# Kernel tuning notes

Measured on AMD Instinct MI355X. Metric: run time of the kernel, lower is better.

Reference implementation:

```python
import jax, jax.numpy as jnp
import numpy as np
from jax import lax

K = 8        # num neighbors (excluding self)
ALPHA = 0.5
EPS = 1e-12


def setup_inputs() -> dict:
    key = jax.random.key(0)
    k1, k2 = jax.random.split(key)
    B, N = 4, 4096
    pred = jax.random.normal(k1, (B, N, 3), dtype=jnp.float32)
    target = jax.random.normal(k2, (B, N, 3), dtype=jnp.float32)
    return {"pred": pred, "target": target}


def _pdist(x):
    # x: [B, N, 3] -> Euclidean distance matrix [B, N, N]
    sq = jnp.sum(x * x, axis=-1)                                # [B, N]
    d2 = sq[:, :, None] + sq[:, None, :] - 2.0 * jnp.einsum('bnd,bmd->bnm', x, x)
    return jnp.sqrt(jnp.maximum(d2, EPS))


def _knn_idx(dist, k):
    # smallest k+1 distances, drop self (first column)
    _, idx = lax.top_k(-dist, k + 1)                            # [B, N, k+1]
    return idx[:, :, 1:]                                        # [B, N, k]


def _gather_points(pts, idx):
    # pts: [B, N, 3], idx: [B, N, k] -> [B, N, k, 3]
    return jax.vmap(lambda p, i: p[i])(pts, idx)


def reference(pred, target):
    # Per-batch losses are means over equal-size point sets, so averaging over
    # (B, N) jointly is identical to the original per-batch loop + /B.
    pred_dist = _pdist(pred)
    target_dist = _pdist(target)
    pred_idx = _knn_idx(pred_dist, K)
    target_idx = _knn_idx(target_dist, K)

    # density: mean kNN distance per point
    pred_density = jnp.mean(jnp.take_along_axis(pred_dist, pred_idx, axis=2), axis=2)
    target_density = jnp.mean(jnp.take_along_axis(target_dist, target_idx, axis=2), axis=2)
    density_loss = jnp.mean((pred_density - target_density) ** 2)

    # direction similarity of normalized neighbor offsets
    pred_nb = _gather_points(pred, pred_idx)                    # [B, N, K, 3]
    target_nb = _gather_points(target, target_idx)
    pred_vec = pred_nb - pred[:, :, None, :]
    target_vec = target_nb - target[:, :, None, :]
    pn = pred_vec / jnp.maximum(jnp.linalg.norm(pred_vec, axis=-1, keepdims=True), EPS)
    tn = target_vec / jnp.maximum(jnp.linalg.norm(target_vec, axis=-1, keepdims=True), EPS)
    direction_loss = 1.0 - jnp.mean(jnp.sum(pn * tn, axis=-1))

    # local covariance (curvature proxy)
    pred_cov = jnp.einsum('bnki,bnkj->bnij', pred_vec, pred_vec) / K    # [B, N, 3, 3]
    target_cov = jnp.einsum('bnki,bnkj->bnij', target_vec, target_vec) / K
    cov_diff = jnp.sqrt(jnp.sum((pred_cov - target_cov) ** 2, axis=(-2, -1)))
    curvature_loss = jnp.mean(cov_diff)

    return density_loss + ALPHA * direction_loss + (1.0 - ALPHA) * curvature_loss
```

## Files before the change

kernel.cpp:

```cpp
#include <hip/hip_runtime.h>
#include <cstdint>
#include <cstddef>

#define NPTS   4096
#define BATCH  4
#define KNN    8
#define NC     16
#define CHN    (NPTS / NC)
#define PD     4
#define EPS_F  1e-12f

__device__ __forceinline__ uint32_t u32min(uint32_t a, uint32_t b) { return a < b ? a : b; }
__device__ __forceinline__ uint32_t u32max(uint32_t a, uint32_t b) { return a > b ? a : b; }

__device__ __forceinline__ uint32_t umed3(uint32_t a, uint32_t b, uint32_t c) {
  uint32_t d;
  asm("v_med3_u32 %0, %1, %2, %3" : "=v"(d) : "v"(a), "v"(b), "v"(c));
  return d;
}

template <int D>
__device__ __forceinline__ void insertD(uint32_t (&loc)[D], uint32_t key) {
  uint32_t prev = loc[0];
  loc[0] = u32min(prev, key);
#pragma unroll
  for (int m = 1; m < D; ++m) {
    const uint32_t cur = loc[m];
    loc[m] = umed3(prev, cur, key);
    prev = cur;
  }
}

template <int D>
__device__ __forceinline__ void scan_chunk(const float4* __restrict__ c4, int j0,
                                           float xix, float xiy, float xiz,
                                           uint32_t (&loc)[D]) {
#pragma unroll
  for (int k = 0; k < D; ++k) loc[k] = 0xFFFFFFFFu;
#pragma unroll 4
  for (int t4 = 0; t4 < CHN / 4; ++t4) {
    const float4 q0 = c4[3 * t4 + 0];
    const float4 q1 = c4[3 * t4 + 1];
    const float4 q2 = c4[3 * t4 + 2];
    const uint32_t jb = (uint32_t)(j0 + 4 * t4);
    {
      const float dx = xix - q0.x, dy = xiy - q0.y, dz = xiz - q0.z;
      const float d2 = fmaf(dx, dx, fmaf(dy, dy, dz * dz));
      insertD<D>(loc, (__float_as_uint(d2) & 0xFFFFF000u) | (jb + 0u));
    }
    {
      const float dx = xix - q0.w, dy = xiy - q1.x, dz = xiz - q1.y;
      const float d2 = fmaf(dx, dx, fmaf(dy, dy, dz * dz));
      insertD<D>(loc, (__float_as_uint(d2) & 0xFFFFF000u) | (jb + 1u));
    }
    {
      const float dx = xix - q1.z, dy = xiy - q1.w, dz = xiz - q2.x;
      const float d2 = fmaf(dx, dx, fmaf(dy, dy, dz * dz));
      insertD<D>(loc, (__float_as_uint(d2) & 0xFFFFF000u) | (jb + 2u));
    }
    {
      const float dx = xix - q2.y, dy = xiy - q2.z, dz = xiz - q2.w;
      const float d2 = fmaf(dx, dx, fmaf(dy, dy, dz * dz));
      insertD<D>(loc, (__float_as_uint(d2) & 0xFFFFF000u) | (jb + 3u));
    }
  }
}

__global__ void __launch_bounds__(256, 4)
knn_partial_k(const float* __restrict__ pred, const float* __restrict__ tgt,
              uint32_t* __restrict__ partial, double* __restrict__ acc,
              uint32_t* __restrict__ ticket) {
  if (blockIdx.x == 0 && threadIdx.x == 0) {
    acc[0] = 0.0; acc[1] = 0.0; acc[2] = 0.0;
    *ticket = 0u;
  }

  int bx = blockIdx.x;
  const int chunk = bx & (NC - 1); bx /= NC;
  const int ig    = bx & 15; bx >>= 4;
  const int b     = bx & 3;  bx >>= 2;
  const int cloud = bx;

  const float* __restrict__ pts = (cloud ? tgt : pred) + (size_t)b * NPTS * 3;
  const int tid = threadIdx.x;
  const int i = ig * 256 + tid;
  const int j0 = chunk * CHN;

  const float xix = pts[3 * i + 0];
  const float xiy = pts[3 * i + 1];
  const float xiz = pts[3 * i + 2];

  const float4* __restrict__ c4 = (const float4*)(pts + 3 * j0);

  uint4 o;
  if (ig == chunk) {
    uint32_t loc[PD + 1];
    scan_chunk<PD + 1>(c4, j0, xix, xiy, xiz, loc);
    o = make_uint4(loc[1], loc[2], loc[3], loc[4]);
  } else {
    uint32_t loc[PD];
    scan_chunk<PD>(c4, j0, xix, xiy, xiz, loc);
    o = make_uint4(loc[0], loc[1], loc[2], loc[3]);
  }
  uint32_t* p = partial +
      ((((size_t)(cloud * BATCH + b) * NC + chunk) * NPTS) + (size_t)i) * PD;
  *(uint4*)p = o;
}

__device__ __forceinline__ void merge2(uint32_t A[KNN], const uint32_t B[KNN]) {
  uint32_t t[KNN];
#pragma unroll
  for (int m = 0; m < KNN; ++m) t[m] = u32min(A[m], B[KNN - 1 - m]);
#define CEU(x, y) { uint32_t lo = u32min(t[x], t[y]); uint32_t hi = u32max(t[x], t[y]); t[x] = lo; t[y] = hi; }
  CEU(0,4) CEU(1,5) CEU(2,6) CEU(3,7)
  CEU(0,2) CEU(1,3) CEU(4,6) CEU(5,7)
  CEU(0,1) CEU(2,3) CEU(4,5) CEU(6,7)
#undef CEU
#pragma unroll
  for (int m = 0; m < KNN; ++m) A[m] = t[m];
}

__device__ __forceinline__ void merge44(const uint2 a0, const uint2 a1,
                                        const uint2 b0, const uint2 b1,
                                        uint32_t s[KNN]) {
  s[0] = a0.x; s[1] = a0.y; s[2] = a1.x; s[3] = a1.y;
  s[4] = b1.y; s[5] = b1.x; s[6] = b0.y; s[7] = b0.x;
#define CEU(x, y) { uint32_t lo = u32min(s[x], s[y]); uint32_t hi = u32max(s[x], s[y]); s[x] = lo; s[y] = hi; }
  CEU(0,4) CEU(1,5) CEU(2,6) CEU(3,7)
  CEU(0,2) CEU(1,3) CEU(4,6) CEU(5,7)
  CEU(0,1) CEU(2,3) CEU(4,5) CEU(6,7)
#undef CEU
}

__device__ __forceinline__ void merge_all(const uint32_t* __restrict__ base,
                                          int i, uint32_t v[KNN]) {
  const size_t stride = (size_t)NPTS * PD;
  const uint32_t* p = base + (size_t)i * PD;
  uint2 q[NC][2];
#pragma unroll
  for (int c = 0; c < NC; ++c) {
    q[c][0] = *(const uint2*)(p + (size_t)c * stride);
    q[c][1] = *(const uint2*)(p + (size_t)c * stride + 2);
  }
  uint32_t L[NC / 2][KNN];
#pragma unroll
  for (int c = 0; c < NC / 2; ++c)
    merge44(q[2 * c][0], q[2 * c][1], q[2 * c + 1][0], q[2 * c + 1][1], L[c]);
  merge2(L[0], L[1]); merge2(L[2], L[3]); merge2(L[4], L[5]); merge2(L[6], L[7]);
  merge2(L[0], L[2]); merge2(L[4], L[6]);
  merge2(L[0], L[4]);
#pragma unroll
  for (int m = 0; m < KNN; ++m) v[m] = L[0][m];
}

__device__ __forceinline__ void cloud_stats(const float* __restrict__ C, int i,
                                            const uint32_t v[KNN],
                                            float& dsum, float cov[6],
                                            float nx[KNN], float ny[KNN], float nz[KNN]) {
  const float qx = C[3 * i], qy = C[3 * i + 1], qz = C[3 * i + 2];
  float jx[KNN], jy[KNN], jz[KNN];
#pragma unroll
  for (int k = 0; k < KNN; ++k) {
    const int j = (int)(v[k] & 0xFFFu);
    jx[k] = C[3 * j]; jy[k] = C[3 * j + 1]; jz[k] = C[3 * j + 2];
  }
  dsum = 0.f;
#pragma unroll
  for (int m = 0; m < 6; ++m) cov[m] = 0.f;
#pragma unroll
  for (int k = 0; k < KNN; ++k) {
    const float ax = jx[k] - qx, ay = jy[k] - qy, az = jz[k] - qz;
    const float d2 = fmaf(ax, ax, fmaf(ay, ay, az * az));
    const float dist = sqrtf(fmaxf(d2, EPS_F));
    const float inv = 1.0f / fmaxf(dist, EPS_F);
    dsum += dist;
    cov[0] += ax * ax; cov[1] += ay * ay; cov[2] += az * az;
    cov[3] += ax * ay; cov[4] += ax * az; cov[5] += ay * az;
    nx[k] = ax * inv; ny[k] = ay * inv; nz[k] = az * inv;
  }
}

__global__ void __launch_bounds__(64, 1)
loss_k(const float* __restrict__ pred, const float* __restrict__ tgt,
       const uint32_t* __restrict__ partial, double* __restrict__ acc,
       uint32_t* __restrict__ ticket, float* __restrict__ out) {
  const int p = blockIdx.x * 64 + threadIdx.x;
  const int b = p >> 12;
  const int i = p & (NPTS - 1);

  const float* __restrict__ P = pred + (size_t)b * NPTS * 3;
  const float* __restrict__ T = tgt  + (size_t)b * NPTS * 3;

  const size_t cstride = (size_t)NC * NPTS * PD;
  uint32_t vp[KNN], vt[KNN];
  merge_all(partial + (size_t)(0 * BATCH + b) * cstride, i, vp);
  merge_all(partial + (size_t)(1 * BATCH + b) * cstride, i, vt);

  float dsp, dst, pcov[6], tcov[6];
  float pnx[KNN], pny[KNN], pnz[KNN], tnx[KNN], tny[KNN], tnz[KNN];
  cloud_stats(P, i, vp, dsp, pcov, pnx, pny, pnz);
  cloud_stats(T, i, vt, dst, tcov, tnx, tny, tnz);

  float sdot = 0.f;
#pragma unroll
  for (int k = 0; k < KNN; ++k)
    sdot += pnx[k] * tnx[k] + pny[k] * tny[k] + pnz[k] * tnz[k];

  const float densp = dsp * (1.0f / KNN);
  const float denst = dst * (1.0f / KNN);
  float e = (densp - denst) * (densp - denst);

  const float dxx = (pcov[0] - tcov[0]) * (1.0f / KNN);
  const float dyy = (pcov[1] - tcov[1]) * (1.0f / KNN);
  const float dzz = (pcov[2] - tcov[2]) * (1.0f / KNN);
  const float dxy = (pcov[3] - tcov[3]) * (1.0f / KNN);
  const float dxz = (pcov[4] - tcov[4]) * (1.0f / KNN);
  const float dyz = (pcov[5] - tcov[5]) * (1.0f / KNN);
  float cfro = sqrtf(dxx * dxx + dyy * dyy + dzz * dzz
                     + 2.0f * (dxy * dxy + dxz * dxz + dyz * dyz));
  float s = sdot;

#pragma unroll
  for (int off = 32; off > 0; off >>= 1) {
    e    += __shfl_down(e, off);
    s    += __shfl_down(s, off);
    cfro += __shfl_down(cfro, off);
  }
  if (threadIdx.x == 0) {
    atomicAdd(&acc[0], (double)e);
    atomicAdd(&acc[1], (double)s);
    atomicAdd(&acc[2], (double)cfro);
    __threadfence();
    const unsigned rank = atomicAdd(ticket, 1u) + 1u;
    if (rank == (unsigned)((BATCH * NPTS) / 64)) {
      __threadfence();
      const double ee = __hip_atomic_load(&acc[0], __ATOMIC_RELAXED, __HIP_MEMORY_SCOPE_AGENT);
      const double ss = __hip_atomic_load(&acc[1], __ATOMIC_RELAXED, __HIP_MEMORY_SCOPE_AGENT);
      const double cc = __hip_atomic_load(&acc[2], __ATOMIC_RELAXED, __HIP_MEMORY_SCOPE_AGENT);
      const double BN = (double)BATCH * (double)NPTS;
      out[0] = (float)(ee / BN + 0.5 * (1.0 - ss / (BN * (double)KNN)) + 0.5 * (cc / BN));
    }
  }
}

extern "C" void kernel_launch(void* const* d_in, const int* in_sizes, int n_in,
                              void* d_out, int out_size, void* d_ws, size_t ws_size,
                              hipStream_t stream) {
  const float* pred = (const float*)d_in[0];
  const float* tgt  = (const float*)d_in[1];
  double* acc = (double*)d_ws;
  uint32_t* ticket = (uint32_t*)((char*)d_ws + 64);
  uint32_t* partial = (uint32_t*)((char*)d_ws + 4096);

  knn_partial_k<<<2 * BATCH * (NPTS / 256) * NC, 256, 0, stream>>>(
      pred, tgt, partial, acc, ticket);
  loss_k<<<(BATCH * NPTS) / 64, 64, 0, stream>>>(
      pred, tgt, partial, acc, ticket, (float*)d_out);
}
```

Baseline: 106.1 us.

## Transpose points to SoA and use packed FP32 math for kNN distances

Adds a pre-pass kernel that converts each point cloud from AoS xyz into separate X/Y/Z arrays in workspace, and moves the accumulator reset into it. The distance scan then loads float4 groups per axis and computes two squared distances at a time with v_pk_add/mul/fma_f32, roughly halving VALU instructions for the distance arithmetic. The cost is an extra kernel launch and a small transpose pass, and the insertion network, likely the dominant cost, is left unchanged.

```diff
diff --git a/kernel.cpp b/kernel.cpp
--- a/kernel.cpp
+++ b/kernel.cpp
@@ -10,6 +10,8 @@
 #define PD     4
 #define EPS_F  1e-12f
 
+typedef float f32x2 __attribute__((ext_vector_type(2)));
+
 __device__ __forceinline__ uint32_t u32min(uint32_t a, uint32_t b) { return a < b ? a : b; }
 __device__ __forceinline__ uint32_t u32max(uint32_t a, uint32_t b) { return a > b ? a : b; }
 
@@ -19,6 +21,22 @@
   return d;
 }
 
+__device__ __forceinline__ f32x2 pk_add(f32x2 a, f32x2 b) {
+  f32x2 d;
+  asm("v_pk_add_f32 %0, %1, %2" : "=v"(d) : "v"(a), "v"(b));
+  return d;
+}
+__device__ __forceinline__ f32x2 pk_mul(f32x2 a, f32x2 b) {
+  f32x2 d;
+  asm("v_pk_mul_f32 %0, %1, %2" : "=v"(d) : "v"(a), "v"(b));
+  return d;
+}
+__device__ __forceinline__ f32x2 pk_fma(f32x2 a, f32x2 b, f32x2 c) {
+  f32x2 d;
+  asm("v_pk_fma_f32 %0, %1, %2, %3" : "=v"(d) : "v"(a), "v"(b), "v"(c));
+  return d;
+}
+
 template <int D>
 __device__ __forceinline__ void insertD(uint32_t (&loc)[D], uint32_t key) {
   uint32_t prev = loc[0];
@@ -31,50 +49,69 @@
   }
 }
 
-template <int D>
-__device__ __forceinline__ void scan_chunk(const float4* __restrict__ c4, int j0,
-                                           float xix, float xiy, float xiz,
-                                           uint32_t (&loc)[D]) {
-#pragma unroll
-  for (int k = 0; k < D; ++k) loc[k] = 0xFFFFFFFFu;
-#pragma unroll 4
-  for (int t4 = 0; t4 < CHN / 4; ++t4) {
-    const float4 q0 = c4[3 * t4 + 0];
-    const float4 q1 = c4[3 * t4 + 1];
-    const float4 q2 = c4[3 * t4 + 2];
-    const uint32_t jb = (uint32_t)(j0 + 4 * t4);
-    {
-      const float dx = xix - q0.x, dy = xiy - q0.y, dz = xiz - q0.z;
-      const float d2 = fmaf(dx, dx, fmaf(dy, dy, dz * dz));
-      insertD<D>(loc, (__float_as_uint(d2) & 0xFFFFF000u) | (jb + 0u));
-    }
-    {
-      const float dx = xix - q0.w, dy = xiy - q1.x, dz = xiz - q1.y;
-      const float d2 = fmaf(dx, dx, fmaf(dy, dy, dz * dz));
-      insertD<D>(loc, (__float_as_uint(d2) & 0xFFFFF000u) | (jb + 1u));
-    }
-    {
-      const float dx = xix - q1.z, dy = xiy - q1.w, dz = xiz - q2.x;
-      const float d2 = fmaf(dx, dx, fmaf(dy, dy, dz * dz));
-      insertD<D>(loc, (__float_as_uint(d2) & 0xFFFFF000u) | (jb + 2u));
-    }
-    {
-      const float dx = xix - q2.y, dy = xiy - q2.z, dz = xiz - q2.w;
-      const float d2 = fmaf(dx, dx, fmaf(dy, dy, dz * dz));
-      insertD<D>(loc, (__float_as_uint(d2) & 0xFFFFF000u) | (jb + 3u));
-    }
-  }
-}
-
-__global__ void __launch_bounds__(256, 4)
-knn_partial_k(const float* __restrict__ pred, const float* __restrict__ tgt,
-              uint32_t* __restrict__ partial, double* __restrict__ acc,
-              uint32_t* __restrict__ ticket) {
+__global__ void __launch_bounds__(256)
+pre_k(const float* __restrict__ pred, const float* __restrict__ tgt,
+      float* __restrict__ soa, double* __restrict__ acc,
+      uint32_t* __restrict__ ticket) {
   if (blockIdx.x == 0 && threadIdx.x == 0) {
     acc[0] = 0.0; acc[1] = 0.0; acc[2] = 0.0;
     *ticket = 0u;
   }
-
+  const int idx = blockIdx.x * 256 + threadIdx.x;
+  const int cb = idx / (3 * NPTS);
+  const int e  = idx - cb * 3 * NPTS;
+  const int axis = e / NPTS;
+  const int j    = e - axis * NPTS;
+  const float* __restrict__ src =
+      (cb >= BATCH ? tgt + (size_t)(cb - BATCH) * NPTS * 3
+                   : pred + (size_t)cb * NPTS * 3);
+  soa[(size_t)cb * 3 * NPTS + (size_t)axis * NPTS + j] = src[3 * j + axis];
+}
+
+template <int D>
+__device__ __forceinline__ void scan_chunk(const float* __restrict__ X,
+                                           const float* __restrict__ Y,
+                                           const float* __restrict__ Z,
+                                           int j0, float xix, float xiy, float xiz,
+                                           uint32_t (&loc)[D]) {
+#pragma unroll
+  for (int k = 0; k < D; ++k) loc[k] = 0xFFFFFFFFu;
+  const f32x2 nqx = {-xix, -xix}, nqy = {-xiy, -xiy}, nqz = {-xiz, -xiz};
+  const float4* __restrict__ X4 = (const float4*)X;
+  const float4* __restrict__ Y4 = (const float4*)Y;
+  const float4* __restrict__ Z4 = (const float4*)Z;
+#pragma unroll 4
+  for (int t = 0; t < CHN / 4; ++t) {
+    const float4 xq = X4[t], yq = Y4[t], zq = Z4[t];
+    const uint32_t jb = (uint32_t)(j0 + 4 * t);
+    {
+      const f32x2 x01 = {xq.x, xq.y}, y01 = {yq.x, yq.y}, z01 = {zq.x, zq.y};
+      const f32x2 dx = pk_add(x01, nqx);
+      const f32x2 dy = pk_add(y01, nqy);
+      const f32x2 dz = pk_add(z01, nqz);
+      f32x2 m = pk_mul(dz, dz);
+      m = pk_fma(dy, dy, m);
+      m = pk_fma(dx, dx, m);
+      insertD<D>(loc, (__float_as_uint(m.x) & 0xFFFFF000u) | (jb + 0u));
+      insertD<D>(loc, (__float_as_uint(m.y) & 0xFFFFF000u) | (jb + 1u));
+    }
+    {
+      const f32x2 x23 = {xq.z, xq.w}, y23 = {yq.z, yq.w}, z23 = {zq.z, zq.w};
+      const f32x2 dx = pk_add(x23, nqx);
+      const f32x2 dy = pk_add(y23, nqy);
+      const f32x2 dz = pk_add(z23, nqz);
+      f32x2 m = pk_mul(dz, dz);
+      m = pk_fma(dy, dy, m);
+      m = pk_fma(dx, dx, m);
+      insertD<D>(loc, (__float_as_uint(m.x) & 0xFFFFF000u) | (jb + 2u));
+      insertD<D>(loc, (__float_as_uint(m.y) & 0xFFFFF000u) | (jb + 3u));
+    }
+  }
+}
+
+__global__ void __launch_bounds__(256, 4)
+knn_partial_k(const float* __restrict__ pred, const float* __restrict__ tgt,
+              const float* __restrict__ soa, uint32_t* __restrict__ partial) {
   int bx = blockIdx.x;
   const int chunk = bx & (NC - 1); bx /= NC;
   const int ig    = bx & 15; bx >>= 4;
@@ -82,6 +119,7 @@
   const int cloud = bx;
 
   const float* __restrict__ pts = (cloud ? tgt : pred) + (size_t)b * NPTS * 3;
+  const float* __restrict__ SO = soa + (size_t)(cloud * BATCH + b) * 3 * NPTS;
   const int tid = threadIdx.x;
   const int i = ig * 256 + tid;
   const int j0 = chunk * CHN;
@@ -90,16 +128,18 @@
   const float xiy = pts[3 * i + 1];
   const float xiz = pts[3 * i + 2];
 
-  const float4* __restrict__ c4 = (const float4*)(pts + 3 * j0);
+  const float* X = SO + 0 * NPTS + j0;
+  const float* Y = SO + 1 * NPTS + j0;
+  const float* Z = SO + 2 * NPTS + j0;
 
   uint4 o;
   if (ig == chunk) {
     uint32_t loc[PD + 1];
-    scan_chunk<PD + 1>(c4, j0, xix, xiy, xiz, loc);
+    scan_chunk<PD + 1>(X, Y, Z, j0, xix, xiy, xiz, loc);
     o = make_uint4(loc[1], loc[2], loc[3], loc[4]);
   } else {
     uint32_t loc[PD];
-    scan_chunk<PD>(c4, j0, xix, xiy, xiz, loc);
+    scan_chunk<PD>(X, Y, Z, j0, xix, xiy, xiz, loc);
     o = make_uint4(loc[0], loc[1], loc[2], loc[3]);
   }
   uint32_t* p = partial +
@@ -250,10 +290,12 @@
   const float* tgt  = (const float*)d_in[1];
   double* acc = (double*)d_ws;
   uint32_t* ticket = (uint32_t*)((char*)d_ws + 64);
-  uint32_t* partial = (uint32_t*)((char*)d_ws + 4096);
-
+  float* soa = (float*)((char*)d_ws + 4096);
+  uint32_t* partial = (uint32_t*)((char*)d_ws + (1 << 20));
+
+  pre_k<<<(2 * BATCH * 3 * NPTS) / 256, 256, 0, stream>>>(pred, tgt, soa, acc, ticket);
   knn_partial_k<<<2 * BATCH * (NPTS / 256) * NC, 256, 0, stream>>>(
-      pred, tgt, partial, acc, ticket);
+      pred, tgt, soa, partial);
   loss_k<<<(BATCH * NPTS) / 64, 64, 0, stream>>>(
       pred, tgt, partial, acc, ticket, (float*)d_out);
 }
```

Result: slower. 121.4 us (+14.4%).
